# Kernel tuning notes

Hardware: AMD Instinct MI355X
Metric: run time of the kernel (lower is better)

## Reference

```python
import jax, jax.numpy as jnp
import numpy as np

EMBED_DIM = 1024
NUM_HEADS = 16
HEAD_DIM = EMBED_DIM // NUM_HEADS


def setup_inputs() -> dict:
    key = jax.random.key(0)
    k_x, k_wqkv, k_bqkv, k_wp, k_bp = jax.random.split(key, 5)
    B, S, D = 2, 2048, EMBED_DIM
    bound_qkv = 1.0 / np.sqrt(D)
    bound_p = 1.0 / np.sqrt(D)
    return {
        "x": jax.random.normal(k_x, (B, S, D), dtype=jnp.float32),
        # torch nn.Linear stores weight as (out, in); keep that layout
        "w_qkv": jax.random.uniform(k_wqkv, (3 * D, D), jnp.float32, -bound_qkv, bound_qkv),
        "b_qkv": jax.random.uniform(k_bqkv, (3 * D,), jnp.float32, -bound_qkv, bound_qkv),
        "w_proj": jax.random.uniform(k_wp, (D, D), jnp.float32, -bound_p, bound_p),
        "b_proj": jax.random.uniform(k_bp, (D,), jnp.float32, -bound_p, bound_p),
    }


def reference(x, w_qkv, b_qkv, w_proj, b_proj):
    B, S, D = x.shape
    H, hd = NUM_HEADS, HEAD_DIM
    qkv = x @ w_qkv.T + b_qkv                      # [B,S,3D]
    qkv = qkv.reshape(B, S, 3, H, hd)
    qkv = jnp.transpose(qkv, (2, 0, 3, 1, 4))       # [3,B,H,S,hd]
    q, k, v = qkv[0], qkv[1], qkv[2]
    scale = 1.0 / np.sqrt(hd)
    scores = jnp.einsum('bhqd,bhkd->bhqk', q, k) * scale  # [B,H,S,S]
    attn = jax.nn.softmax(scores, axis=-1)
    out = jnp.einsum('bhqk,bhkd->bhqd', attn, v)    # [B,H,S,hd]
    out = jnp.transpose(out, (0, 2, 1, 3)).reshape(B, S, D)
    return out @ w_proj.T + b_proj
```

## Files before the change

### kernel.cpp

```cpp
#include <hip/hip_runtime.h>
#include <hip/hip_bf16.h>
#include <math.h>


typedef __bf16 bf16_t;
typedef __bf16 bf16x8 __attribute__((ext_vector_type(8)));
typedef __bf16 bf16x4v __attribute__((ext_vector_type(4)));
typedef float f32x4 __attribute__((ext_vector_type(4)));
typedef float f32x16 __attribute__((ext_vector_type(16)));

#define B_ 2
#define S_ 2048
#define D_ 1024
#define H_ 16
#define HD_ 64
#define QSCALE 0.18033688011112042f

__device__ __forceinline__ void load_lds16(const void* g, void* s) {
  __builtin_amdgcn_global_load_lds((__attribute__((address_space(1))) unsigned int*)g,
                                   (__attribute__((address_space(3))) unsigned int*)s,
                                   16, 0, 0);
}

__global__ void tobf16_all(const float* __restrict__ x, const float* __restrict__ wq,
                           const float* __restrict__ wp, bf16_t* __restrict__ xb,
                           bf16_t* __restrict__ wqb, bf16_t* __restrict__ wpb) {
  int bid = blockIdx.x;
  const float* in;
  bf16_t* out;
  int base;
  if (bid < 4096) { in = x; out = xb; base = bid; }
  else if (bid < 7168) { in = wq; out = wqb; base = bid - 4096; }
  else { in = wp; out = wpb; base = bid - 7168; }
  int i = base * 256 + threadIdx.x;
  float4 v = ((const float4*)in)[i];
  bf16x4v o;
  o[0] = (bf16_t)v.x; o[1] = (bf16_t)v.y; o[2] = (bf16_t)v.z; o[3] = (bf16_t)v.w;
  ((bf16x4v*)out)[i] = o;
}

template <int EPI, int BN>
__global__ __launch_bounds__(256, 2) void gemm_bt(
    const bf16_t* __restrict__ A, const bf16_t* __restrict__ Bm,
    const float* __restrict__ bias,
    bf16_t* __restrict__ qb, bf16_t* __restrict__ kb, bf16_t* __restrict__ vtb,
    float* __restrict__ outf) {
  constexpr int NI = BN / 32;
  constexpr int BUF = 8192 + BN * 64;
  __shared__ __align__(16) char smem[2 * BUF];
  const int tid = threadIdx.x;
  const int w = tid >> 6, lane = tid & 63;
  const int wm = w >> 1, wn = w & 1;
  const int quad = lane >> 4, l15 = lane & 15;
  const int m0 = blockIdx.y * 128, n0 = blockIdx.x * BN;

  auto stage = [&](int kt, int bb) {
    char* bA = smem + bb * BUF;
    char* bB = bA + 8192;
#pragma unroll
    for (int i = 0; i < 2; i++) {
      int ub = w * 128 + i * 64;
      int u = ub + lane;
      int r = u >> 2, c = (u & 3) ^ ((r >> 1) & 3);
      load_lds16(A + (size_t)(m0 + r) * 1024 + kt + c * 8, bA + (size_t)ub * 16);
    }
#pragma unroll
    for (int i = 0; i < BN / 64; i++) {
      int ub = w * (BN / 64) * 64 + i * 64;
      int u = ub + lane;
      int r = u >> 2, c = (u & 3) ^ ((r >> 1) & 3);
      load_lds16(Bm + (size_t)(n0 + r) * 1024 + kt + c * 8, bB + (size_t)ub * 16);
    }
  };

  f32x4 acc[4][NI];
#pragma unroll
  for (int mi = 0; mi < 4; mi++)
#pragma unroll
    for (int ni = 0; ni < NI; ni++) acc[mi][ni] = (f32x4){0.f, 0.f, 0.f, 0.f};

  stage(0, 0);

  for (int it = 0; it < 32; it++) {
    __syncthreads();
    if (it < 31) stage((it + 1) * 32, (it + 1) & 1);
    const bf16_t* bA = (const bf16_t*)(smem + (it & 1) * BUF);
    const bf16_t* bB = (const bf16_t*)(smem + (it & 1) * BUF + 8192);

    bf16x8 af[4], bfr[NI];
#pragma unroll
    for (int mi = 0; mi < 4; mi++) {
      int r = wm * 64 + mi * 16 + l15;
      af[mi] = *(const bf16x8*)(bA + (r * 4 + (quad ^ ((r >> 1) & 3))) * 8);
    }
#pragma unroll
    for (int ni = 0; ni < NI; ni++) {
      int r = wn * (BN / 2) + ni * 16 + l15;
      bfr[ni] = *(const bf16x8*)(bB + (r * 4 + (quad ^ ((r >> 1) & 3))) * 8);
    }
#pragma unroll
    for (int mi = 0; mi < 4; mi++)
#pragma unroll
      for (int ni = 0; ni < NI; ni++)
        acc[mi][ni] = __builtin_amdgcn_mfma_f32_16x16x32_bf16(af[mi], bfr[ni], acc[mi][ni], 0, 0, 0);
  }

#pragma unroll
  for (int mi = 0; mi < 4; mi++) {
#pragma unroll
    for (int ni = 0; ni < NI; ni++) {
      int n = n0 + wn * (BN / 2) + ni * 16 + l15;
      float bv = bias[n];
#pragma unroll
      for (int r = 0; r < 4; r++) {
        int m = m0 + wm * 64 + mi * 16 + quad * 4 + r;
        float v = acc[mi][ni][r] + bv;
        if (EPI == 0) {
          int t = n >> 10;
          int rr = n & 1023;
          int hh = rr >> 6, d = rr & 63;
          int bb = m >> 11, s = m & 2047;
          size_t bh = (size_t)(bb * H_ + hh);
          if (t == 0)
            qb[(bh * S_ + s) * HD_ + d] = (bf16_t)(v * QSCALE);
          else if (t == 1)
            kb[(bh * S_ + s) * HD_ + d] = (bf16_t)v;
          else
            vtb[(bh * HD_ + d) * S_ + s] = (bf16_t)v;
        } else {
          outf[(size_t)m * 1024 + n] = v;
        }
      }
    }
  }
}

__global__ __launch_bounds__(256, 2) void attn(
    const bf16_t* __restrict__ qb, const bf16_t* __restrict__ kb,
    const bf16_t* __restrict__ vtb, bf16_t* __restrict__ ob) {
  __shared__ __align__(16) char smem[49152];
  const int tid = threadIdx.x, w = tid >> 6, lane = tid & 63;
  const int h2 = lane >> 5, l31 = lane & 31;
  const int gid = blockIdx.x;
  const int g = gid & 7, k_ = gid >> 3;
  const int bh = g * 4 + (k_ >> 4);
  const int qt = k_ & 15;
  const int b = bh >> 4, h = bh & 15;
  const size_t base = (size_t)bh * S_ * HD_;
  const size_t vbase = (size_t)bh * HD_ * S_;
  const int q0 = qt * 128;
  char* Pw = smem + 32768 + w * 4096;

  bf16x8 aq[4];
#pragma unroll
  for (int ks = 0; ks < 4; ks++)
    aq[ks] = *(const bf16x8*)(qb + base + (size_t)(q0 + w * 32 + l31) * 64 + ks * 16 + h2 * 8);

  auto stage = [&](int kv0, int bb) {
    char* bK = smem + bb * 16384;
    char* bV = bK + 8192;
#pragma unroll
    for (int i = 0; i < 2; i++) {
      int ub = i * 256 + w * 64;
      int u = ub + lane;
      int rk = u >> 3, ck = (u & 7) ^ (rk & 7);
      load_lds16(kb + base + (size_t)(kv0 + rk) * 64 + ck * 8, bK + (size_t)ub * 16);
      int rv = u >> 3, cv = (u & 7) ^ (rv & 7);
      load_lds16(vtb + vbase + (size_t)rv * S_ + kv0 + cv * 8, bV + (size_t)ub * 16);
    }
  };

  f32x16 acc_o[2];
#pragma unroll
  for (int dt = 0; dt < 2; dt++)
#pragma unroll
    for (int i = 0; i < 16; i++) acc_o[dt][i] = 0.f;
  float l_part[16];
#pragma unroll
  for (int i = 0; i < 16; i++) l_part[i] = 0.f;

  stage(0, 0);

  for (int j = 0; j < 32; j++) {
    __syncthreads();
    if (j < 31) stage((j + 1) * 64, (j + 1) & 1);
    const bf16_t* bK = (const bf16_t*)(smem + (j & 1) * 16384);
    const bf16_t* bV = bK + 4096;

    f32x16 s_acc[2];
#pragma unroll
    for (int nt = 0; nt < 2; nt++)
#pragma unroll
      for (int i = 0; i < 16; i++) s_acc[nt][i] = 0.f;
#pragma unroll
    for (int ks = 0; ks < 4; ks++) {
#pragma unroll
      for (int nt = 0; nt < 2; nt++) {
        int r = nt * 32 + l31;
        bf16x8 bk = *(const bf16x8*)(bK + (r * 8 + ((ks * 2 + h2) ^ (r & 7))) * 8);
        s_acc[nt] = __builtin_amdgcn_mfma_f32_32x32x16_bf16(aq[ks], bk, s_acc[nt], 0, 0, 0);
      }
    }

#pragma unroll
    for (int reg = 0; reg < 16; reg++) {
      int rr = (reg & 3) + 8 * (reg >> 2) + 4 * h2;
      float p0 = exp2f(s_acc[0][reg]);
      float p1 = exp2f(s_acc[1][reg]);
      l_part[reg] += p0 + p1;
      int u0 = ((l31 >> 3) ^ (rr & 7));
      int u1 = (((l31 >> 3) + 4) ^ (rr & 7));
      *(bf16_t*)(Pw + rr * 128 + u0 * 16 + (l31 & 7) * 2) = (bf16_t)p0;
      *(bf16_t*)(Pw + rr * 128 + u1 * 16 + (l31 & 7) * 2) = (bf16_t)p1;
    }

#pragma unroll
    for (int ks = 0; ks < 4; ks++) {
      bf16x8 ap = *(const bf16x8*)(Pw + l31 * 128 + (((ks * 2 + h2) ^ (l31 & 7)) * 16));
#pragma unroll
      for (int dt = 0; dt < 2; dt++) {
        int r = dt * 32 + l31;
        bf16x8 bv = *(const bf16x8*)(bV + (r * 8 + ((ks * 2 + h2) ^ (r & 7))) * 8);
        acc_o[dt] = __builtin_amdgcn_mfma_f32_32x32x16_bf16(ap, bv, acc_o[dt], 0, 0, 0);
      }
    }
  }

  float inv_l[16];
#pragma unroll
  for (int reg = 0; reg < 16; reg++) {
    float v = l_part[reg];
    v += __shfl_xor(v, 1);
    v += __shfl_xor(v, 2);
    v += __shfl_xor(v, 4);
    v += __shfl_xor(v, 8);
    v += __shfl_xor(v, 16);
    inv_l[reg] = 1.0f / v;
  }

#pragma unroll
  for (int dt = 0; dt < 2; dt++)
#pragma unroll
    for (int reg = 0; reg < 16; reg++) {
      int rr = (reg & 3) + 8 * (reg >> 2) + 4 * h2;
      int q = q0 + w * 32 + rr;
      int d = dt * 32 + l31;
      float v = acc_o[dt][reg] * inv_l[reg];
      ob[((size_t)b * S_ + q) * D_ + h * HD_ + d] = (bf16_t)v;
    }
}

extern "C" void kernel_launch(void* const* d_in, const int* in_sizes, int n_in,
                              void* d_out, int out_size, void* d_ws, size_t ws_size,
                              hipStream_t stream) {
  const float* x = (const float*)d_in[0];
  const float* w_qkv = (const float*)d_in[1];
  const float* b_qkv = (const float*)d_in[2];
  const float* w_proj = (const float*)d_in[3];
  const float* b_proj = (const float*)d_in[4];
  float* out = (float*)d_out;

  char* ws = (char*)d_ws;
  size_t off = 0;
  bf16_t* xb = (bf16_t*)(ws + off); off += (size_t)4096 * 1024 * 2;
  bf16_t* wqkvb = (bf16_t*)(ws + off); off += (size_t)3072 * 1024 * 2;
  bf16_t* wpb = (bf16_t*)(ws + off); off += (size_t)1024 * 1024 * 2;
  bf16_t* qb = (bf16_t*)(ws + off); off += (size_t)4096 * 1024 * 2;
  bf16_t* kb = (bf16_t*)(ws + off); off += (size_t)4096 * 1024 * 2;
  bf16_t* vtb = (bf16_t*)(ws + off); off += (size_t)4096 * 1024 * 2;
  bf16_t* ob = xb;

  tobf16_all<<<8192, 256, 0, stream>>>(x, w_qkv, w_proj, xb, wqkvb, wpb);
  gemm_bt<0, 128><<<dim3(24, 32), 256, 0, stream>>>(xb, wqkvb, b_qkv, qb, kb, vtb, nullptr);
  attn<<<512, 256, 0, stream>>>(qb, kb, vtb, ob);
  gemm_bt<1, 64><<<dim3(16, 32), 256, 0, stream>>>(ob, wpb, b_proj, nullptr, nullptr, nullptr, out);
}
```

Baseline: 207.7 us.

## Deepen GEMM K-tile to 64, halve attention block size, pack P stores

The GEMM now stages a K=64 tile per iteration with an 8-chunk XOR swizzle, halving the number of barriers and loop iterations at the cost of twice the LDS per stage. The attention kernel moves to 128-thread blocks covering 64 queries each, launched as 1024 blocks, with less shared memory per block. The K rows are interleaved so each lane's two S columns sit next to each other, which lets P be written to LDS as packed bf16 pairs instead of scalar stores. These changes give more parallelism and fewer LDS transactions, but K/V staging is now shared by fewer queries, so global traffic per block rises.

```diff
diff --git a/kernel.cpp b/kernel.cpp
--- a/kernel.cpp
+++ b/kernel.cpp
@@ -6,6 +6,7 @@
 typedef __bf16 bf16_t;
 typedef __bf16 bf16x8 __attribute__((ext_vector_type(8)));
 typedef __bf16 bf16x4v __attribute__((ext_vector_type(4)));
+typedef __bf16 bf16x2 __attribute__((ext_vector_type(2)));
 typedef float f32x4 __attribute__((ext_vector_type(4)));
 typedef float f32x16 __attribute__((ext_vector_type(16)));
 
@@ -46,7 +47,7 @@
     bf16_t* __restrict__ qb, bf16_t* __restrict__ kb, bf16_t* __restrict__ vtb,
     float* __restrict__ outf) {
   constexpr int NI = BN / 32;
-  constexpr int BUF = 8192 + BN * 64;
+  constexpr int BUF = (128 + BN) * 128;
   __shared__ __align__(16) char smem[2 * BUF];
   const int tid = threadIdx.x;
   const int w = tid >> 6, lane = tid & 63;
@@ -56,19 +57,19 @@
 
   auto stage = [&](int kt, int bb) {
     char* bA = smem + bb * BUF;
-    char* bB = bA + 8192;
-#pragma unroll
-    for (int i = 0; i < 2; i++) {
-      int ub = w * 128 + i * 64;
+    char* bB = bA + 16384;
+#pragma unroll
+    for (int i = 0; i < 4; i++) {
+      int ub = w * 256 + i * 64;
       int u = ub + lane;
-      int r = u >> 2, c = (u & 3) ^ ((r >> 1) & 3);
+      int r = u >> 3, c = (u & 7) ^ (r & 7);
       load_lds16(A + (size_t)(m0 + r) * 1024 + kt + c * 8, bA + (size_t)ub * 16);
     }
 #pragma unroll
-    for (int i = 0; i < BN / 64; i++) {
-      int ub = w * (BN / 64) * 64 + i * 64;
+    for (int i = 0; i < BN / 32; i++) {
+      int ub = w * (BN / 32) * 64 + i * 64;
       int u = ub + lane;
-      int r = u >> 2, c = (u & 3) ^ ((r >> 1) & 3);
+      int r = u >> 3, c = (u & 7) ^ (r & 7);
       load_lds16(Bm + (size_t)(n0 + r) * 1024 + kt + c * 8, bB + (size_t)ub * 16);
     }
   };
@@ -81,28 +82,31 @@
 
   stage(0, 0);
 
-  for (int it = 0; it < 32; it++) {
+  for (int it = 0; it < 16; it++) {
     __syncthreads();
-    if (it < 31) stage((it + 1) * 32, (it + 1) & 1);
+    if (it < 15) stage((it + 1) * 64, (it + 1) & 1);
     const bf16_t* bA = (const bf16_t*)(smem + (it & 1) * BUF);
-    const bf16_t* bB = (const bf16_t*)(smem + (it & 1) * BUF + 8192);
-
-    bf16x8 af[4], bfr[NI];
-#pragma unroll
-    for (int mi = 0; mi < 4; mi++) {
-      int r = wm * 64 + mi * 16 + l15;
-      af[mi] = *(const bf16x8*)(bA + (r * 4 + (quad ^ ((r >> 1) & 3))) * 8);
-    }
-#pragma unroll
-    for (int ni = 0; ni < NI; ni++) {
-      int r = wn * (BN / 2) + ni * 16 + l15;
-      bfr[ni] = *(const bf16x8*)(bB + (r * 4 + (quad ^ ((r >> 1) & 3))) * 8);
-    }
-#pragma unroll
-    for (int mi = 0; mi < 4; mi++)
-#pragma unroll
-      for (int ni = 0; ni < NI; ni++)
-        acc[mi][ni] = __builtin_amdgcn_mfma_f32_16x16x32_bf16(af[mi], bfr[ni], acc[mi][ni], 0, 0, 0);
+    const bf16_t* bB = (const bf16_t*)(smem + (it & 1) * BUF + 16384);
+
+#pragma unroll
+    for (int kk = 0; kk < 2; kk++) {
+      bf16x8 af[4], bfr[NI];
+#pragma unroll
+      for (int mi = 0; mi < 4; mi++) {
+        int r = wm * 64 + mi * 16 + l15;
+        af[mi] = *(const bf16x8*)(bA + (r * 8 + ((kk * 4 + quad) ^ (r & 7))) * 8);
+      }
+#pragma unroll
+      for (int ni = 0; ni < NI; ni++) {
+        int r = wn * (BN / 2) + ni * 16 + l15;
+        bfr[ni] = *(const bf16x8*)(bB + (r * 8 + ((kk * 4 + quad) ^ (r & 7))) * 8);
+      }
+#pragma unroll
+      for (int mi = 0; mi < 4; mi++)
+#pragma unroll
+        for (int ni = 0; ni < NI; ni++)
+          acc[mi][ni] = __builtin_amdgcn_mfma_f32_16x16x32_bf16(af[mi], bfr[ni], acc[mi][ni], 0, 0, 0);
+    }
   }
 
 #pragma unroll
@@ -135,20 +139,20 @@
   }
 }
 
-__global__ __launch_bounds__(256, 2) void attn(
+__global__ __launch_bounds__(128, 2) void attn(
     const bf16_t* __restrict__ qb, const bf16_t* __restrict__ kb,
     const bf16_t* __restrict__ vtb, bf16_t* __restrict__ ob) {
-  __shared__ __align__(16) char smem[49152];
+  __shared__ __align__(16) char smem[40960];
   const int tid = threadIdx.x, w = tid >> 6, lane = tid & 63;
   const int h2 = lane >> 5, l31 = lane & 31;
   const int gid = blockIdx.x;
   const int g = gid & 7, k_ = gid >> 3;
-  const int bh = g * 4 + (k_ >> 4);
-  const int qt = k_ & 15;
+  const int bh = g * 4 + (k_ >> 5);
+  const int qt = k_ & 31;
   const int b = bh >> 4, h = bh & 15;
   const size_t base = (size_t)bh * S_ * HD_;
   const size_t vbase = (size_t)bh * HD_ * S_;
-  const int q0 = qt * 128;
+  const int q0 = qt * 64;
   char* Pw = smem + 32768 + w * 4096;
 
   bf16x8 aq[4];
@@ -160,10 +164,10 @@
     char* bK = smem + bb * 16384;
     char* bV = bK + 8192;
 #pragma unroll
-    for (int i = 0; i < 2; i++) {
-      int ub = i * 256 + w * 64;
+    for (int i = 0; i < 4; i++) {
+      int ub = w * 256 + i * 64;
       int u = ub + lane;
-      int rk = u >> 3, ck = (u & 7) ^ (rk & 7);
+      int rk = u >> 3, ck = (u & 7) ^ ((rk >> 1) & 7);
       load_lds16(kb + base + (size_t)(kv0 + rk) * 64 + ck * 8, bK + (size_t)ub * 16);
       int rv = u >> 3, cv = (u & 7) ^ (rv & 7);
       load_lds16(vtb + vbase + (size_t)rv * S_ + kv0 + cv * 8, bV + (size_t)ub * 16);
@@ -196,8 +200,8 @@
     for (int ks = 0; ks < 4; ks++) {
 #pragma unroll
       for (int nt = 0; nt < 2; nt++) {
-        int r = nt * 32 + l31;
-        bf16x8 bk = *(const bf16x8*)(bK + (r * 8 + ((ks * 2 + h2) ^ (r & 7))) * 8);
+        int r = 2 * l31 + nt;
+        bf16x8 bk = *(const bf16x8*)(bK + (r * 8 + ((ks * 2 + h2) ^ (l31 & 7))) * 8);
         s_acc[nt] = __builtin_amdgcn_mfma_f32_32x32x16_bf16(aq[ks], bk, s_acc[nt], 0, 0, 0);
       }
     }
@@ -208,10 +212,10 @@
       float p0 = exp2f(s_acc[0][reg]);
       float p1 = exp2f(s_acc[1][reg]);
       l_part[reg] += p0 + p1;
-      int u0 = ((l31 >> 3) ^ (rr & 7));
-      int u1 = (((l31 >> 3) + 4) ^ (rr & 7));
-      *(bf16_t*)(Pw + rr * 128 + u0 * 16 + (l31 & 7) * 2) = (bf16_t)p0;
-      *(bf16_t*)(Pw + rr * 128 + u1 * 16 + (l31 & 7) * 2) = (bf16_t)p1;
+      bf16x2 pk;
+      pk[0] = (bf16_t)p0;
+      pk[1] = (bf16_t)p1;
+      *(bf16x2*)(Pw + rr * 128 + (((l31 >> 2) ^ (rr & 7)) * 16) + (l31 & 3) * 4) = pk;
     }
 
 #pragma unroll
@@ -272,6 +276,6 @@
 
   tobf16_all<<<8192, 256, 0, stream>>>(x, w_qkv, w_proj, xb, wqkvb, wpb);
   gemm_bt<0, 128><<<dim3(24, 32), 256, 0, stream>>>(xb, wqkvb, b_qkv, qb, kb, vtb, nullptr);
-  attn<<<512, 256, 0, stream>>>(qb, kb, vtb, ob);
+  attn<<<1024, 128, 0, stream>>>(qb, kb, vtb, ob);
   gemm_bt<1, 64><<<dim3(16, 32), 256, 0, stream>>>(ob, wpb, b_proj, nullptr, nullptr, nullptr, out);
 }
```

New measurement: 219.6 us. 5.7% more time.
